# Performance work log

Measured on AMD Instinct MI355X. Metric: run time of the kernel, lower is better.

The kernel has to match this reference:

```python
import jax, jax.numpy as jnp
import numpy as np

BANDWIDTH = 8.0  # gaussian kernel std


def setup_inputs() -> dict:
    key = jax.random.key(0)
    k1, k2 = jax.random.split(key)
    B, N, M, D = 2, 8192, 8192, 64
    return {
        "points": jax.random.normal(k1, (B, N, D), dtype=jnp.float32),
        "ref_points": jax.random.normal(k2, (B, M, D), dtype=jnp.float32),
    }


def reference(points, ref_points):
    # Squared pairwise distances via the |x|^2 + |y|^2 - 2<x,y> expansion
    # (same math as ((x_i - y_j)**2).sum(-1), avoids a [B,N,M,D] intermediate).
    sq_p = jnp.sum(points * points, axis=-1)          # [B,N]
    sq_r = jnp.sum(ref_points * ref_points, axis=-1)  # [B,M]
    s_ij = (sq_p[:, :, None] + sq_r[:, None, :]
            - 2.0 * jnp.einsum('bnd,bmd->bnm', points, ref_points))  # [B,N,M]
    # Gaussian kernel
    k_ij = jnp.exp(s_ij * (-1.0 / (2.0 * BANDWIDTH ** 2)))  # [B,N,M]
    # Weighted mean of reference points (nominator.sum(2) / k_ij.sum(2))
    nominator = jnp.einsum('bnm,bmd->bnd', k_ij, ref_points)  # [B,N,D]
    denominator = jnp.sum(k_ij, axis=-1, keepdims=True)       # [B,N,1]
    return nominator / denominator
```

## Files before the change

kernel.cpp:

```cpp
#include <hip/hip_runtime.h>

constexpr int B_ = 2, N_ = 8192, M_ = 8192, Dd = 64;
constexpr int TN = 128;
constexpr int TM = 64;
constexpr int SPLIT = 8;
constexpr int MCHUNK = M_ / SPLIT;
constexpr int NCHUNKS = MCHUNK / TM;
constexpr int NT = N_ / TN;
constexpr float LOG2E   = 1.4426950408889634f;
constexpr float SCALE_S = LOG2E / 64.0f;
constexpr float SCALE_N = -LOG2E / 128.0f;

using s16x8 = __attribute__((ext_vector_type(8))) short;
using f32x4 = __attribute__((ext_vector_type(4))) float;
using f32x2v = __attribute__((ext_vector_type(2))) float;
using bf16x2 = __attribute__((ext_vector_type(2))) __bf16;

#if defined(__has_builtin)
#if __has_builtin(__builtin_amdgcn_exp2f)
#define EXP2(x) __builtin_amdgcn_exp2f(x)
#endif
#endif
#ifndef EXP2
#define EXP2(x) exp2f(x)
#endif

__device__ __forceinline__ unsigned pk2(float lo, float hi) {
  f32x2v f;
  f[0] = lo;
  f[1] = hi;
  bf16x2 h = __builtin_convertvector(f, bf16x2);
  return __builtin_bit_cast(unsigned, h);
}
__device__ __forceinline__ f32x4 mfma16(s16x8 a, s16x8 b, f32x4 c) {
  return __builtin_amdgcn_mfma_f32_16x16x32_bf16(a, b, c, 0, 0, 0);
}
__device__ __forceinline__ float dot4(float4 f) {
  return f.x * f.x + f.y * f.y + f.z * f.z + f.w * f.w;
}


__global__ __launch_bounds__(256, 3) void msflash_kernel(
    const float* __restrict__ pts, const float* __restrict__ ref,
    float* __restrict__ num_acc, float* __restrict__ den_acc) {
  __shared__ unsigned short ldsY2[2][TM][72];
  __shared__ unsigned short ldsYT2[2][Dd][64];
  __shared__ unsigned short ldsPp[4][32][64];
  __shared__ float lds_an2[TN];
  __shared__ float lds_bm2[2][TM];

  const int tid  = threadIdx.x;
  const int w    = tid >> 6;
  const int lane = tid & 63;
  const int l15  = lane & 15, quad = lane >> 4;
  const int ytsw = quad + (l15 & 7);
  const int psw  = l15 & 7;

  const int s  = blockIdx.x & (SPLIT - 1);
  const int r  = blockIdx.x >> 3;
  const int bb = r / NT;
  const int nt_ = r % NT;
  const int n0 = nt_ * TN;
  const int m_begin = s * MCHUNK;

  const int rowl_s = tid >> 2, q_s = tid & 3;
  const float* ybase = ref + ((size_t)bb * M_ + m_begin + rowl_s) * Dd + q_s * 16;
  float4 fv0, fv1, fv2, fv3;

  auto loadfv = [&](int cc) {
    const float* yp = ybase + (size_t)cc * TM * Dd;
    fv0 = ((const float4*)yp)[0];
    fv1 = ((const float4*)yp)[1];
    fv2 = ((const float4*)yp)[2];
    fv3 = ((const float4*)yp)[3];
  };
  auto stage = [&](int bp) {
    unsigned pkd[8] = {pk2(fv0.x, fv0.y), pk2(fv0.z, fv0.w),
                       pk2(fv1.x, fv1.y), pk2(fv1.z, fv1.w),
                       pk2(fv2.x, fv2.y), pk2(fv2.z, fv2.w),
                       pk2(fv3.x, fv3.y), pk2(fv3.z, fv3.w)};
    float sq = dot4(fv0) + dot4(fv1) + dot4(fv2) + dot4(fv3);
    sq += __shfl_xor(sq, 1);
    sq += __shfl_xor(sq, 2);
    if (q_s == 0) lds_bm2[bp][rowl_s] = sq * SCALE_N;
    uint4* dv = (uint4*)&ldsY2[bp][rowl_s][q_s * 16];
    dv[0] = make_uint4(pkd[0], pkd[1], pkd[2], pkd[3]);
    dv[1] = make_uint4(pkd[4], pkd[5], pkd[6], pkd[7]);
    const int tsw = (rowl_s >> 3) + 2 * q_s;
    const int mlo = rowl_s & 7;
#pragma unroll
    for (int j = 0; j < 8; j++) {
      const int d0 = q_s * 16 + 2 * j;
      const int c0 = (tsw + ((2 * j) & 7)) & 7;
      const int c1 = (tsw + ((2 * j + 1) & 7)) & 7;
      ldsYT2[bp][d0][(c0 << 3) + mlo]     = (unsigned short)pkd[j];
      ldsYT2[bp][d0 + 1][(c1 << 3) + mlo] = (unsigned short)(pkd[j] >> 16);
    }
  };

  loadfv(0);
  unsigned short (*ldsX)[72] = (unsigned short (*)[72]) & ldsY2[0][0][0];
  {
    const int rowl = tid >> 1, half = tid & 1;
    const float* gp = pts + ((size_t)bb * N_ + n0 + rowl) * Dd + half * 32;
    float sq = 0.f;
    unsigned pkd[16];
#pragma unroll
    for (int i = 0; i < 8; i++) {
      float4 f = ((const float4*)gp)[i];
      sq += dot4(f);
      pkd[2 * i + 0] = pk2(f.x, f.y);
      pkd[2 * i + 1] = pk2(f.z, f.w);
    }
    sq += __shfl_xor(sq, 1);
    if (half == 0) lds_an2[rowl] = sq * SCALE_N;
    uint4* dv = (uint4*)&ldsX[rowl][half * 32];
#pragma unroll
    for (int i = 0; i < 4; i++)
      dv[i] = make_uint4(pkd[4 * i], pkd[4 * i + 1], pkd[4 * i + 2], pkd[4 * i + 3]);
  }
  __syncthreads();

  s16x8 bx[2][2];
  float anr_s[2];
#pragma unroll
  for (int rt = 0; rt < 2; rt++) {
#pragma unroll
    for (int ks = 0; ks < 2; ks++)
      bx[rt][ks] = *(const s16x8*)&ldsX[w * 32 + rt * 16 + l15][ks * 32 + quad * 8];
    anr_s[rt] = lds_an2[w * 32 + rt * 16 + l15];
  }
  __syncthreads();

  stage(0);
  loadfv(1);
  __syncthreads();

  f32x4 o[2][4], den[2];
#pragma unroll
  for (int rt = 0; rt < 2; rt++) {
    den[rt] = f32x4{0.f, 0.f, 0.f, 0.f};
#pragma unroll
    for (int dt = 0; dt < 4; dt++) o[rt][dt] = f32x4{0.f, 0.f, 0.f, 0.f};
  }
  s16x8 ones;
#pragma unroll
  for (int j = 0; j < 8; j++) ones[j] = (l15 == 0) ? (short)0x3F80 : (short)0;

  int p = 0;
  for (int c = 0; c < NCHUNKS; ++c) {
    f32x4 sf[2][4];
#pragma unroll
    for (int ct = 0; ct < 4; ct++) {
      s16x8 a0 = *(const s16x8*)&ldsY2[p][ct * 16 + l15][quad * 8];
      s16x8 a1 = *(const s16x8*)&ldsY2[p][ct * 16 + l15][32 + quad * 8];
#pragma unroll
      for (int rt = 0; rt < 2; rt++) {
        f32x4 acc = f32x4{0.f, 0.f, 0.f, 0.f};
        acc = mfma16(a0, bx[rt][0], acc);
        acc = mfma16(a1, bx[rt][1], acc);
        sf[rt][ct] = acc;
      }
    }
#pragma unroll
    for (int ct = 0; ct < 4; ct++) {
      f32x4 bm = *(const f32x4*)&lds_bm2[p][ct * 16 + quad * 4];
#pragma unroll
      for (int rt = 0; rt < 2; rt++) {
        float e0 = EXP2(sf[rt][ct][0] * SCALE_S + (anr_s[rt] + bm[0]));
        float e1 = EXP2(sf[rt][ct][1] * SCALE_S + (anr_s[rt] + bm[1]));
        float e2 = EXP2(sf[rt][ct][2] * SCALE_S + (anr_s[rt] + bm[2]));
        float e3 = EXP2(sf[rt][ct][3] * SCALE_S + (anr_s[rt] + bm[3]));
        const int oW = (2 * ct + (quad >> 1) + psw) & 7;
        *(uint2*)&ldsPp[w][rt * 16 + l15][(oW << 3) + (quad & 1) * 4] =
            make_uint2(pk2(e0, e1), pk2(e2, e3));
      }
    }
    s16x8 pf[2][2];
#pragma unroll
    for (int rt = 0; rt < 2; rt++)
#pragma unroll
      for (int ks = 0; ks < 2; ks++) {
        const int oR = (4 * ks + quad + psw) & 7;
        pf[rt][ks] = *(const s16x8*)&ldsPp[w][rt * 16 + l15][oR << 3];
      }
#pragma unroll
    for (int dt = 0; dt < 4; dt++) {
      const unsigned short* yt = &ldsYT2[p][dt * 16 + l15][0];
      s16x8 a0 = *(const s16x8*)&yt[((ytsw + 2 * dt) & 7) << 3];
      s16x8 a1 = *(const s16x8*)&yt[((ytsw + 4 + 2 * dt) & 7) << 3];
#pragma unroll
      for (int rt = 0; rt < 2; rt++) {
        o[rt][dt] = mfma16(a0, pf[rt][0], o[rt][dt]);
        o[rt][dt] = mfma16(a1, pf[rt][1], o[rt][dt]);
      }
    }
#pragma unroll
    for (int rt = 0; rt < 2; rt++) {
      den[rt] = mfma16(ones, pf[rt][0], den[rt]);
      den[rt] = mfma16(ones, pf[rt][1], den[rt]);
    }
    stage(p ^ 1);
    loadfv(c + 2 < NCHUNKS ? c + 2 : NCHUNKS - 1);
    __syncthreads();
    p ^= 1;
  }

  float* ldsO = (float*)&ldsY2[0][0][0] + (size_t)w * 1152;
  float* nb = num_acc + ((size_t)bb * N_ + n0) * Dd;
#pragma unroll
  for (int rt = 0; rt < 2; rt++) {
#pragma unroll
    for (int dt = 0; dt < 4; dt++) {
      const int base = l15 * 66 + dt * 16 + quad * 4;
      *(float2*)&ldsO[base + 0] = make_float2(o[rt][dt][0], o[rt][dt][1]);
      *(float2*)&ldsO[base + 2] = make_float2(o[rt][dt][2], o[rt][dt][3]);
    }
    const int nrow = w * 32 + rt * 16;
#pragma unroll
    for (int rr = 0; rr < 16; rr++) {
      float v = ldsO[rr * 66 + lane];
      atomicAdd(&nb[(size_t)(nrow + rr) * Dd + lane], v);
    }
    if (quad == 0)
      atomicAdd(&den_acc[(size_t)bb * N_ + n0 + nrow + l15], den[rt][0]);
  }
}

__global__ __launch_bounds__(256) void msdiv_kernel(
    const float* __restrict__ num, const float* __restrict__ den,
    float* __restrict__ out) {
  const int i = blockIdx.x * 256 + threadIdx.x;
  float4 v = ((const float4*)num)[i];
  const float inv = 1.0f / den[i >> 4];
  ((float4*)out)[i] = make_float4(v.x * inv, v.y * inv, v.z * inv, v.w * inv);
}

extern "C" void kernel_launch(void* const* d_in, const int* in_sizes, int n_in,
                              void* d_out, int out_size, void* d_ws, size_t ws_size,
                              hipStream_t stream) {
  const float* pts = (const float*)d_in[0];
  const float* ref = (const float*)d_in[1];
  float* out = (float*)d_out;
  float* num = (float*)d_ws;
  float* den = num + (size_t)B_ * N_ * Dd;
  const size_t acc_bytes = ((size_t)B_ * N_ * Dd + (size_t)B_ * N_) * sizeof(float);

  hipMemsetAsync(d_ws, 0, acc_bytes, stream);
  msflash_kernel<<<dim3(B_ * NT * SPLIT), dim3(256), 0, stream>>>(pts, ref, num, den);
  const int tot4 = B_ * N_ * Dd / 4;
  msdiv_kernel<<<dim3(tot4 / 256), dim3(256), 0, stream>>>(num, den, out);
}
```

Measured before the change: 127.9 us.

## Shrink per-wave P scratch in LDS and raise occupancy to four blocks

Splits the exp/pack stage over two k-halves so each wave only needs a 16x32 bf16 scratch tile for P instead of 32x64. The second GEMM is interleaved with exp production per k-half. lds_an2 is aliased into the new scratch, and launch bounds move from 3 to 4 blocks per CU. This cuts LDS use and register pressure to raise occupancy. The cost is more LDS write/read round trips per chunk and possible register spills under the tighter launch bound.

```diff
diff --git a/kernel.cpp b/kernel.cpp
--- a/kernel.cpp
+++ b/kernel.cpp
@@ -40,13 +40,12 @@
 }
 
 
-__global__ __launch_bounds__(256, 3) void msflash_kernel(
+__global__ __launch_bounds__(256, 4) void msflash_kernel(
     const float* __restrict__ pts, const float* __restrict__ ref,
     float* __restrict__ num_acc, float* __restrict__ den_acc) {
   __shared__ unsigned short ldsY2[2][TM][72];
   __shared__ unsigned short ldsYT2[2][Dd][64];
-  __shared__ unsigned short ldsPp[4][32][64];
-  __shared__ float lds_an2[TN];
+  __shared__ unsigned short ldsQ[4][16][32];
   __shared__ float lds_bm2[2][TM];
 
   const int tid  = threadIdx.x;
@@ -54,7 +53,7 @@
   const int lane = tid & 63;
   const int l15  = lane & 15, quad = lane >> 4;
   const int ytsw = quad + (l15 & 7);
-  const int psw  = l15 & 7;
+  const int psm  = l15 & 3;
 
   const int s  = blockIdx.x & (SPLIT - 1);
   const int r  = blockIdx.x >> 3;
@@ -100,6 +99,7 @@
 
   loadfv(0);
   unsigned short (*ldsX)[72] = (unsigned short (*)[72]) & ldsY2[0][0][0];
+  float* lds_an2 = (float*)&ldsQ[0][0][0];
   {
     const int rowl = tid >> 1, half = tid & 1;
     const float* gp = pts + ((size_t)bb * N_ + n0 + rowl) * Dd + half * 32;
@@ -163,42 +163,35 @@
       }
     }
 #pragma unroll
-    for (int ct = 0; ct < 4; ct++) {
-      f32x4 bm = *(const f32x4*)&lds_bm2[p][ct * 16 + quad * 4];
+    for (int ks = 0; ks < 2; ks++) {
+      f32x4 bmA = *(const f32x4*)&lds_bm2[p][(2 * ks + 0) * 16 + quad * 4];
+      f32x4 bmB = *(const f32x4*)&lds_bm2[p][(2 * ks + 1) * 16 + quad * 4];
+      s16x8 pf01[2];
 #pragma unroll
       for (int rt = 0; rt < 2; rt++) {
-        float e0 = EXP2(sf[rt][ct][0] * SCALE_S + (anr_s[rt] + bm[0]));
-        float e1 = EXP2(sf[rt][ct][1] * SCALE_S + (anr_s[rt] + bm[1]));
-        float e2 = EXP2(sf[rt][ct][2] * SCALE_S + (anr_s[rt] + bm[2]));
-        float e3 = EXP2(sf[rt][ct][3] * SCALE_S + (anr_s[rt] + bm[3]));
-        const int oW = (2 * ct + (quad >> 1) + psw) & 7;
-        *(uint2*)&ldsPp[w][rt * 16 + l15][(oW << 3) + (quad & 1) * 4] =
-            make_uint2(pk2(e0, e1), pk2(e2, e3));
+#pragma unroll
+        for (int cl = 0; cl < 2; cl++) {
+          const f32x4& bm = cl ? bmB : bmA;
+          const f32x4& sv = sf[rt][2 * ks + cl];
+          float e0 = EXP2(sv[0] * SCALE_S + (anr_s[rt] + bm[0]));
+          float e1 = EXP2(sv[1] * SCALE_S + (anr_s[rt] + bm[1]));
+          float e2 = EXP2(sv[2] * SCALE_S + (anr_s[rt] + bm[2]));
+          float e3 = EXP2(sv[3] * SCALE_S + (anr_s[rt] + bm[3]));
+          const int ch = ((2 * cl + (quad >> 1)) ^ psm);
+          *(uint2*)&ldsQ[w][l15][ch * 8 + (quad & 1) * 4] =
+              make_uint2(pk2(e0, e1), pk2(e2, e3));
+        }
+        pf01[rt] = *(const s16x8*)&ldsQ[w][l15][(quad ^ psm) * 8];
       }
-    }
-    s16x8 pf[2][2];
-#pragma unroll
-    for (int rt = 0; rt < 2; rt++)
-#pragma unroll
-      for (int ks = 0; ks < 2; ks++) {
-        const int oR = (4 * ks + quad + psw) & 7;
-        pf[rt][ks] = *(const s16x8*)&ldsPp[w][rt * 16 + l15][oR << 3];
+#pragma unroll
+      for (int dt = 0; dt < 4; dt++) {
+        const unsigned short* yt = &ldsYT2[p][dt * 16 + l15][0];
+        s16x8 a = *(const s16x8*)&yt[((ytsw + 4 * ks + 2 * dt) & 7) << 3];
+        o[0][dt] = mfma16(a, pf01[0], o[0][dt]);
+        o[1][dt] = mfma16(a, pf01[1], o[1][dt]);
       }
-#pragma unroll
-    for (int dt = 0; dt < 4; dt++) {
-      const unsigned short* yt = &ldsYT2[p][dt * 16 + l15][0];
-      s16x8 a0 = *(const s16x8*)&yt[((ytsw + 2 * dt) & 7) << 3];
-      s16x8 a1 = *(const s16x8*)&yt[((ytsw + 4 + 2 * dt) & 7) << 3];
-#pragma unroll
-      for (int rt = 0; rt < 2; rt++) {
-        o[rt][dt] = mfma16(a0, pf[rt][0], o[rt][dt]);
-        o[rt][dt] = mfma16(a1, pf[rt][1], o[rt][dt]);
-      }
-    }
-#pragma unroll
-    for (int rt = 0; rt < 2; rt++) {
-      den[rt] = mfma16(ones, pf[rt][0], den[rt]);
-      den[rt] = mfma16(ones, pf[rt][1], den[rt]);
+      den[0] = mfma16(ones, pf01[0], den[0]);
+      den[1] = mfma16(ones, pf01[1], den[1]);
     }
     stage(p ^ 1);
     loadfv(c + 2 < NCHUNKS ? c + 2 : NCHUNKS - 1);
```

Result: slower. 157.0 us (+22.8%).
